# Kernel tuning notes

Hardware: AMD Instinct MI355X
Metric: run time of the kernel (lower is better)

The kernel has to match this reference:

```python
import jax, jax.numpy as jnp
import numpy as np

N, E, D = 50000, 600000, 128
NEG_SLOPE = 0.2

def setup_inputs() -> dict:
    key = jax.random.key(0)
    ks = jax.random.split(key, 12)
    s = 1.0 / np.sqrt(D)
    return {
        "x": jax.random.normal(ks[0], (N, D), jnp.float32),
        "edge_index": jax.random.randint(ks[1], (2, E), 0, N),
        "edge_attr": jax.random.normal(ks[2], (E, D), jnp.float32),
        "ln1_g": jnp.ones((D,), jnp.float32),
        "ln1_b": jnp.zeros((D,), jnp.float32),
        "W_lin": jax.random.normal(ks[3], (D, D), jnp.float32) * s,
        "att_src": jax.random.normal(ks[4], (D,), jnp.float32) * s,
        "att_dst": jax.random.normal(ks[5], (D,), jnp.float32) * s,
        "W_edge": jax.random.normal(ks[6], (D, D), jnp.float32) * s,
        "att_edge": jax.random.normal(ks[7], (D,), jnp.float32) * s,
        "gat_bias": jnp.zeros((D,), jnp.float32),
        "ln2_g": jnp.ones((D,), jnp.float32),
        "ln2_b": jnp.zeros((D,), jnp.float32),
        "W1": jax.random.normal(ks[8], (D, 4 * D), jnp.float32) * s,
        "b1": jnp.zeros((4 * D,), jnp.float32),
        "W2": jax.random.normal(ks[9], (4 * D, D), jnp.float32) * (1.0 / np.sqrt(4 * D)),
        "b2": jnp.zeros((D,), jnp.float32),
    }


def _layernorm(x, g, b, eps=1e-5):
    mu = jnp.mean(x, axis=-1, keepdims=True)
    var = jnp.mean(jnp.square(x - mu), axis=-1, keepdims=True)
    return (x - mu) * jax.lax.rsqrt(var + eps) * g + b


def _gat_conv(x, edge_index, edge_attr, W_lin, att_src, att_dst, W_edge, att_edge, gat_bias):
    # PyG GATConv, heads=1, concat=False, add_self_loops=False, edge_dim=D
    src, dst = edge_index[0], edge_index[1]
    h = x @ W_lin                      # [N, D] shared src/dst projection
    a_src = h @ att_src                # [N]
    a_dst = h @ att_dst                # [N]
    a_edge = (edge_attr @ W_edge) @ att_edge  # [E]
    alpha = a_src[src] + a_dst[dst] + a_edge  # [E]
    alpha = jnp.where(alpha > 0, alpha, NEG_SLOPE * alpha)  # leaky_relu(0.2)
    # segment softmax over destination nodes
    m = jax.ops.segment_max(alpha, dst, num_segments=N)
    m = jnp.where(jnp.isfinite(m), m, 0.0)
    ex = jnp.exp(alpha - m[dst])
    denom = jax.ops.segment_sum(ex, dst, num_segments=N)
    coef = ex / jnp.maximum(denom[dst], 1e-16)
    # weighted scatter-aggregation of source messages
    out = jax.ops.segment_sum(coef[:, None] * h[src], dst, num_segments=N)
    return out + gat_bias


def reference(x, edge_index, edge_attr, ln1_g, ln1_b, W_lin, att_src, att_dst,
              W_edge, att_edge, gat_bias, ln2_g, ln2_b, W1, b1, W2, b2):
    # pre-norm + GAT message passing + residual (dropout = eval identity)
    xn = _layernorm(x, ln1_g, ln1_b)
    x = x + _gat_conv(xn, edge_index, edge_attr, W_lin, att_src, att_dst,
                      W_edge, att_edge, gat_bias)
    # pre-norm + FFN + residual
    xn = _layernorm(x, ln2_g, ln2_b)
    ffn = jax.nn.relu(xn @ W1 + b1) @ W2 + b2
    return x + ffn
```

## Files before the change

### kernel.cpp

```cpp
#include <hip/hip_runtime.h>

#define D 128
#define NEG_SLOPE 0.2f

typedef __attribute__((ext_vector_type(8))) short short8;
typedef __attribute__((ext_vector_type(4))) float f32x4;

__device__ __forceinline__ float wred_sum(float v){
#pragma unroll
  for (int m = 32; m; m >>= 1) v += __shfl_xor(v, m);
  return v;
}
__device__ __forceinline__ int wred_sumi(int v){
#pragma unroll
  for (int m = 32; m; m >>= 1) v += __shfl_xor(v, m);
  return v;
}
__device__ __forceinline__ float wred_max(float v){
#pragma unroll
  for (int m = 32; m; m >>= 1) v = fmaxf(v, __shfl_xor(v, m));
  return v;
}
__device__ __forceinline__ unsigned short bf16r(float f){
  unsigned int u = __float_as_uint(f);
  u += 0x7fffu + ((u >> 16) & 1u);
  return (unsigned short)(u >> 16);
}
__device__ __forceinline__ float bf2f(unsigned int hi16){
  return __uint_as_float(hi16 << 16);
}

__global__ void k_prep0(const float* __restrict__ W_lin, const float* __restrict__ W1,
                        const float* __restrict__ W2, const float* __restrict__ W_edge,
                        const float* __restrict__ att_edge,
                        unsigned short* __restrict__ Wlt, unsigned short* __restrict__ W1t,
                        unsigned short* __restrict__ W2t, float* __restrict__ we,
                        int* __restrict__ cnt, int N){
  int t = blockIdx.x * blockDim.x + threadIdx.x;
  if (t < N) cnt[t] = 0;
  if (t < 128 * 128){
    int c = t >> 7, k = t & 127;
    Wlt[t] = bf16r(W_lin[k * 128 + c]);
  } else if (t < 128 * 128 + 512 * 128){
    int u = t - 128 * 128; int c = u >> 7, k = u & 127;
    W1t[u] = bf16r(W1[k * 512 + c]);
  } else if (t < 128 * 128 + 512 * 128 + 128 * 512){
    int u = t - (128 * 128 + 512 * 128); int c = u >> 9, k = u & 511;
    W2t[u] = bf16r(W2[k * 128 + c]);
  } else {
    int u = t - (128 * 128 + 512 * 128 + 128 * 512);
    if (u < 128){
      float s = 0.f;
      for (int j = 0; j < 128; ++j) s += W_edge[u * 128 + j] * att_edge[j];
      we[u] = s;
    }
  }
}

__global__ __launch_bounds__(256) void k_hgemm(const float* __restrict__ x,
                                               const unsigned short* __restrict__ Wlt,
                                               const float* __restrict__ ln1_g,
                                               const float* __restrict__ ln1_b,
                                               const float* __restrict__ att_src,
                                               const float* __restrict__ att_dst,
                                               const int* __restrict__ ei,
                                               unsigned short* __restrict__ hq,
                                               float* __restrict__ asrc,
                                               float* __restrict__ adst,
                                               int* __restrict__ cnt, int N, int E){
  int wid = threadIdx.x >> 6, lane = threadIdx.x & 63;
  int rb = blockIdx.x * 64 + wid * 16;
  int row = rb + (lane & 15);
  int rowc = row < N ? row : N - 1;
  int ksub = (lane >> 4) * 8;
  float v[4][8];
#pragma unroll
  for (int kb = 0; kb < 4; ++kb){
    float4 p0 = *(const float4*)(x + (size_t)rowc * 128 + kb * 32 + ksub);
    float4 p1 = *(const float4*)(x + (size_t)rowc * 128 + kb * 32 + ksub + 4);
    v[kb][0] = p0.x; v[kb][1] = p0.y; v[kb][2] = p0.z; v[kb][3] = p0.w;
    v[kb][4] = p1.x; v[kb][5] = p1.y; v[kb][6] = p1.z; v[kb][7] = p1.w;
  }
  float s = 0.f;
#pragma unroll
  for (int kb = 0; kb < 4; ++kb)
#pragma unroll
    for (int j = 0; j < 8; ++j) s += v[kb][j];
  s += __shfl_xor(s, 16); s += __shfl_xor(s, 32);
  float mu = s * (1.0f / 128.f);
  float q = 0.f;
#pragma unroll
  for (int kb = 0; kb < 4; ++kb)
#pragma unroll
    for (int j = 0; j < 8; ++j){ float d = v[kb][j] - mu; q += d * d; }
  q += __shfl_xor(q, 16); q += __shfl_xor(q, 32);
  float rstd = rsqrtf(q * (1.0f / 128.f) + 1e-5f);
  short8 a[4];
#pragma unroll
  for (int kb = 0; kb < 4; ++kb){
    float4 g0 = *(const float4*)(ln1_g + kb * 32 + ksub);
    float4 g1 = *(const float4*)(ln1_g + kb * 32 + ksub + 4);
    float4 b0 = *(const float4*)(ln1_b + kb * 32 + ksub);
    float4 b1 = *(const float4*)(ln1_b + kb * 32 + ksub + 4);
    float gg[8] = {g0.x,g0.y,g0.z,g0.w,g1.x,g1.y,g1.z,g1.w};
    float bb[8] = {b0.x,b0.y,b0.z,b0.w,b1.x,b1.y,b1.z,b1.w};
#pragma unroll
    for (int j = 0; j < 8; ++j)
      a[kb][j] = (short)bf16r((v[kb][j] - mu) * rstd * gg[j] + bb[j]);
  }
  f32x4 acc[8];
#pragma unroll
  for (int ct = 0; ct < 8; ++ct) acc[ct] = (f32x4){0.f, 0.f, 0.f, 0.f};
#pragma unroll
  for (int ct = 0; ct < 8; ++ct){
    int col = ct * 16 + (lane & 15);
#pragma unroll
    for (int kb = 0; kb < 4; ++kb){
      short8 bf = *(const short8*)(Wlt + (size_t)col * 128 + kb * 32 + ksub);
      acc[ct] = __builtin_amdgcn_mfma_f32_16x16x32_bf16(a[kb], bf, acc[ct], 0, 0, 0);
    }
  }
  int r0 = rb + (lane >> 4) * 4;
#pragma unroll
  for (int ct = 0; ct < 8; ++ct){
    int col = ct * 16 + (lane & 15);
#pragma unroll
    for (int j = 0; j < 4; ++j){
      int r = r0 + j;
      if (r < N) hq[(size_t)r * 128 + col] = bf16r(acc[ct][j]);
    }
  }
  float as_v[8], ad_v[8];
#pragma unroll
  for (int ct = 0; ct < 8; ++ct){
    int col = ct * 16 + (lane & 15);
    as_v[ct] = att_src[col];
    ad_v[ct] = att_dst[col];
  }
  float ps[4] = {0.f, 0.f, 0.f, 0.f}, pd[4] = {0.f, 0.f, 0.f, 0.f};
#pragma unroll
  for (int ct = 0; ct < 8; ++ct)
#pragma unroll
    for (int j = 0; j < 4; ++j){
      ps[j] += acc[ct][j] * as_v[ct];
      pd[j] += acc[ct][j] * ad_v[ct];
    }
#pragma unroll
  for (int m = 1; m < 16; m <<= 1)
#pragma unroll
    for (int j = 0; j < 4; ++j){
      ps[j] += __shfl_xor(ps[j], m);
      pd[j] += __shfl_xor(pd[j], m);
    }
  if ((lane & 15) == 0){
#pragma unroll
    for (int j = 0; j < 4; ++j){
      int r = r0 + j;
      if (r < N){ asrc[r] = ps[j]; adst[r] = pd[j]; }
    }
  }
  int t = blockIdx.x * blockDim.x + threadIdx.x;
  int stride = gridDim.x * blockDim.x;
  for (int e = t; e < E; e += stride) atomicAdd(&cnt[ei[E + e]], 1);
}

__global__ void k_escan(const int* __restrict__ cnt, int* __restrict__ start,
                        int* __restrict__ cursor, int N){
  int b = blockIdx.x, t = threadIdx.x;
  int base = b * 256;
  int acc = 0;
  for (int i = t; i < base; i += 256) acc += cnt[i];
  acc = wred_sumi(acc);
  __shared__ int wsum[4];
  if ((t & 63) == 0) wsum[t >> 6] = acc;
  __syncthreads();
  int s_off = wsum[0] + wsum[1] + wsum[2] + wsum[3];
  int i = base + t;
  int c = (i < N) ? cnt[i] : 0;
  __shared__ int sd[256];
  sd[t] = c;
  __syncthreads();
  for (int off = 1; off < 256; off <<= 1){
    int vv = (t >= off) ? sd[t - off] : 0;
    __syncthreads();
    sd[t] += vv;
    __syncthreads();
  }
  int st = s_off + sd[t] - c;
  if (i <= N) start[i] = st;
  if (i < N) cursor[i] = st;
}

__global__ void k_edge_scatter(const float* __restrict__ ea, const int* __restrict__ ei,
                               const float* __restrict__ we, const float* __restrict__ asrc,
                               const float* __restrict__ adst, int* __restrict__ cursor,
                               int2* __restrict__ esa, int E){
  int gw = (blockIdx.x * blockDim.x + threadIdx.x) >> 6;
  int lane = threadIdx.x & 63;
  int e = gw * 2 + (lane >> 5);
  int li = lane & 31;
  if (e >= E) return;
  float4 v = *(const float4*)(ea + (size_t)e * 128 + li * 4);
  float4 w = *(const float4*)(we + li * 4);
  float s = v.x * w.x + v.y * w.y + v.z * w.z + v.w * w.w;
#pragma unroll
  for (int m = 16; m; m >>= 1) s += __shfl_xor(s, m);
  if (li == 0){
    int sn = ei[e], dn = ei[E + e];
    float al = asrc[sn] + adst[dn] + s;
    al = al > 0.f ? al : NEG_SLOPE * al;
    int slot = atomicAdd(&cursor[dn], 1);
    esa[slot] = make_int2(sn, __float_as_int(al));
  }
}

__global__ void k_agg(const float* __restrict__ x, const unsigned short* __restrict__ hq,
                      const int* __restrict__ start, const int2* __restrict__ esa,
                      const float* __restrict__ gat_bias,
                      const float* __restrict__ g2, const float* __restrict__ b2,
                      float* __restrict__ out, unsigned short* __restrict__ xn2q, int N){
  int n = (blockIdx.x * blockDim.x + threadIdx.x) >> 6;
  int lane = threadIdx.x & 63;
  if (n >= N) return;
  int beg = start[n], end = start[n + 1];
  float m = -1e30f, ds = 0.f, a0 = 0.f, a1 = 0.f;
  for (int cb = beg; cb < end; cb += 64){
    int k = end - cb; if (k > 64) k = 64;
    int2 ev = (cb + lane < end) ? esa[cb + lane] : make_int2(0, (int)0xFF800000u);
    float al = __int_as_float(ev.y);
    float mn = fmaxf(m, wred_max(al));
    float sc = __expf(m - mn);
    ds *= sc; a0 *= sc; a1 *= sc;
    m = mn;
    float ex = __expf(al - m);
    int j = 0;
    for (; j + 4 <= k; j += 4){
      float e0 = __shfl(ex, j), e1 = __shfl(ex, j + 1);
      float e2 = __shfl(ex, j + 2), e3 = __shfl(ex, j + 3);
      int s0 = __shfl(ev.x, j), s1 = __shfl(ev.x, j + 1);
      int s2 = __shfl(ev.x, j + 2), s3 = __shfl(ev.x, j + 3);
      unsigned int h0 = *(const unsigned int*)(hq + (size_t)s0 * 128 + lane * 2);
      unsigned int h1 = *(const unsigned int*)(hq + (size_t)s1 * 128 + lane * 2);
      unsigned int h2 = *(const unsigned int*)(hq + (size_t)s2 * 128 + lane * 2);
      unsigned int h3 = *(const unsigned int*)(hq + (size_t)s3 * 128 + lane * 2);
      ds += e0 + e1 + e2 + e3;
      a0 += e0 * bf2f(h0 & 0xffffu) + e1 * bf2f(h1 & 0xffffu)
          + e2 * bf2f(h2 & 0xffffu) + e3 * bf2f(h3 & 0xffffu);
      a1 += e0 * bf2f(h0 >> 16) + e1 * bf2f(h1 >> 16)
          + e2 * bf2f(h2 >> 16) + e3 * bf2f(h3 >> 16);
    }
    for (; j < k; ++j){
      float ej = __shfl(ex, j);
      int sj = __shfl(ev.x, j);
      unsigned int hv = *(const unsigned int*)(hq + (size_t)sj * 128 + lane * 2);
      ds += ej;
      a0 += ej * bf2f(hv & 0xffffu);
      a1 += ej * bf2f(hv >> 16);
    }
  }
  float inv = (end > beg) ? 1.f / fmaxf(ds, 1e-16f) : 0.f;
  a0 *= inv; a1 *= inv;
  float2 xv  = *(const float2*)(x + (size_t)n * 128 + lane * 2);
  float2 gbv = *(const float2*)(gat_bias + lane * 2);
  float r0 = xv.x + a0 + gbv.x;
  float r1 = xv.y + a1 + gbv.y;
  float mu = wred_sum(r0 + r1) * (1.0f / 128.f);
  float d0 = r0 - mu, d1 = r1 - mu;
  float var = wred_sum(d0 * d0 + d1 * d1) * (1.0f / 128.f);
  float rstd = rsqrtf(var + 1e-5f);
  float2 gv = *(const float2*)(g2 + lane * 2);
  float2 bv = *(const float2*)(b2 + lane * 2);
  float o0 = d0 * rstd * gv.x + bv.x;
  float o1 = d1 * rstd * gv.y + bv.y;
  *(float2*)(out + (size_t)n * 128 + lane * 2) = make_float2(r0, r1);
  unsigned int p = (unsigned int)bf16r(o0) | ((unsigned int)bf16r(o1) << 16);
  *(unsigned int*)(xn2q + (size_t)n * 128 + lane * 2) = p;
}

__global__ __launch_bounds__(512) void k_ffn(const unsigned short* __restrict__ xn2q,
                                             const unsigned short* __restrict__ W1t,
                                             const unsigned short* __restrict__ W2t,
                                             const float* __restrict__ b1,
                                             const float* __restrict__ b2,
                                             float* __restrict__ out, int N){
  __shared__ unsigned short hid[64 * 512];
  int wid = threadIdx.x >> 6, lane = threadIdx.x & 63;
  int rg = wid >> 1;
  int ch = wid & 1;
  int rb = blockIdx.x * 64;
  int lr = rg * 16;
  int arow = rb + lr + (lane & 15);
  int arowc = arow < N ? arow : N - 1;
  int ksub = (lane >> 4) * 8;
  short8 a[4];
#pragma unroll
  for (int kb = 0; kb < 4; ++kb)
    a[kb] = *(const short8*)(xn2q + (size_t)arowc * 128 + kb * 32 + ksub);
  int lr0 = lr + (lane >> 4) * 4;
#pragma unroll 4
  for (int ct = 0; ct < 16; ++ct){
    int col = ch * 256 + ct * 16 + (lane & 15);
    f32x4 acc = {0.f, 0.f, 0.f, 0.f};
#pragma unroll
    for (int kb = 0; kb < 4; ++kb){
      short8 bf = *(const short8*)(W1t + (size_t)col * 128 + kb * 32 + ksub);
      acc = __builtin_amdgcn_mfma_f32_16x16x32_bf16(a[kb], bf, acc, 0, 0, 0);
    }
    float bias = b1[col];
#pragma unroll
    for (int j = 0; j < 4; ++j){
      float v = acc[j] + bias;
      v = v > 0.f ? v : 0.f;
      int row = lr0 + j;
      int byte = (col * 2) ^ ((row & 7) << 4);
      *(unsigned short*)((char*)hid + row * 1024 + byte) = bf16r(v);
    }
  }
  __syncthreads();
  f32x4 acc2[4];
#pragma unroll
  for (int ct = 0; ct < 4; ++ct) acc2[ct] = (f32x4){0.f, 0.f, 0.f, 0.f};
  int arow2 = lr + (lane & 15);
#pragma unroll 2
  for (int kb = 0; kb < 16; ++kb){
    int kbyte = (kb * 32 + ksub) * 2;
    int sb = kbyte ^ ((arow2 & 7) << 4);
    short8 af = *(const short8*)((const char*)hid + arow2 * 1024 + sb);
#pragma unroll
    for (int ct = 0; ct < 4; ++ct){
      int col = ch * 64 + ct * 16 + (lane & 15);
      short8 bf = *(const short8*)(W2t + (size_t)col * 512 + kb * 32 + ksub);
      acc2[ct] = __builtin_amdgcn_mfma_f32_16x16x32_bf16(af, bf, acc2[ct], 0, 0, 0);
    }
  }
  int r0 = rb + lr0;
#pragma unroll
  for (int ct = 0; ct < 4; ++ct){
    int col = ch * 64 + ct * 16 + (lane & 15);
    float bias = b2[col];
#pragma unroll
    for (int j = 0; j < 4; ++j){
      int row = r0 + j;
      if (row < N) out[(size_t)row * 128 + col] += acc2[ct][j] + bias;
    }
  }
}

extern "C" void kernel_launch(void* const* d_in, const int* in_sizes, int n_in,
                              void* d_out, int out_size, void* d_ws, size_t ws_size,
                              hipStream_t stream){
  const float* x        = (const float*)d_in[0];
  const int*   ei       = (const int*)  d_in[1];
  const float* ea       = (const float*)d_in[2];
  const float* ln1_g    = (const float*)d_in[3];
  const float* ln1_b    = (const float*)d_in[4];
  const float* W_lin    = (const float*)d_in[5];
  const float* att_src  = (const float*)d_in[6];
  const float* att_dst  = (const float*)d_in[7];
  const float* W_edge   = (const float*)d_in[8];
  const float* att_edge = (const float*)d_in[9];
  const float* gat_bias = (const float*)d_in[10];
  const float* ln2_g    = (const float*)d_in[11];
  const float* ln2_b    = (const float*)d_in[12];
  const float* W1       = (const float*)d_in[13];
  const float* b1       = (const float*)d_in[14];
  const float* W2       = (const float*)d_in[15];
  const float* b2       = (const float*)d_in[16];

  const int N = in_sizes[0] / 128;
  const int E = in_sizes[2] / 128;
  float* out = (float*)d_out;

  char* p = (char*)d_ws;
  auto carve = [&](size_t bytes) -> char* {
    char* r = p; p += (bytes + 255) & ~(size_t)255; return r;
  };
  unsigned short* hq       = (unsigned short*)carve((size_t)N * 128 * 2);
  unsigned short* xn2q     = (unsigned short*)carve((size_t)N * 128 * 2);
  float*          asrc     = (float*)carve((size_t)N * 4);
  float*          adst     = (float*)carve((size_t)N * 4);
  int2*           esa      = (int2*)carve((size_t)E * 8);
  int*            cnt      = (int*)carve((size_t)N * 4);
  int*            cursor   = (int*)carve((size_t)N * 4);
  int*            start    = (int*)carve((size_t)(N + 1) * 4);
  unsigned short* Wlt      = (unsigned short*)carve(128 * 128 * 2);
  unsigned short* W1t      = (unsigned short*)carve(512 * 128 * 2);
  unsigned short* W2t      = (unsigned short*)carve(128 * 512 * 2);
  float*          we       = (float*)carve(128 * 4);

  k_prep0<<<(128*128 + 512*128 + 128*512 + 128 + 255) / 256, 256, 0, stream>>>(
      W_lin, W1, W2, W_edge, att_edge, Wlt, W1t, W2t, we, cnt, N);
  k_hgemm<<<(N + 63) / 64, 256, 0, stream>>>(x, Wlt, ln1_g, ln1_b, att_src, att_dst, ei,
                                             hq, asrc, adst, cnt, N, E);
  k_escan<<<N / 256 + 1, 256, 0, stream>>>(cnt, start, cursor, N);
  k_edge_scatter<<<(E + 7) / 8, 256, 0, stream>>>(ea, ei, we, asrc, adst, cursor, esa, E);
  k_agg<<<(N + 3) / 4, 256, 0, stream>>>(x, hq, start, esa, gat_bias, ln2_g, ln2_b,
                                         out, xn2q, N);
  k_ffn<<<(N + 63) / 64, 512, 0, stream>>>(xn2q, W1t, W2t, b1, b2, out, N);
}
```

Measured before the change: 344.9 us.

## Fuse all GAT layer stages into one cooperative persistent kernel

Replaces the six-kernel pipeline with a single cooperative-launch persistent kernel that uses grid-wide syncs between phases: weight prep, edge-logit GEMV overlapped with the node GEMM on split block groups, a scan, the edge scatter, aggregation and the FFN. The goal is to remove launch gaps and tail idling between small kernels. The cost is a fixed grid of 256 blocks, a serial per-chunk scan prefix, and several grid barriers. Aggregation also switches to a two-pass max-then-sum softmax using half-warps per node, and the fallback k_agg gets the same two-pass loop.

After: 510.4 us. +48.0%, slower.

```diff
diff --git a/kernel.cpp b/kernel.cpp
--- a/kernel.cpp
+++ b/kernel.cpp
@@ -1,7 +1,13 @@
 #include <hip/hip_runtime.h>
+#include <hip/hip_cooperative_groups.h>
+
+namespace cg = cooperative_groups;
 
 #define D 128
 #define NEG_SLOPE 0.2f
+#define GRID 256
+#define BLK 512
+#define EB 160
 
 typedef __attribute__((ext_vector_type(8))) short short8;
 typedef __attribute__((ext_vector_type(4))) float f32x4;
@@ -29,6 +35,340 @@
 __device__ __forceinline__ float bf2f(unsigned int hi16){
   return __uint_as_float(hi16 << 16);
 }
+
+struct P {
+  const float *x; const int *ei; const float *ea;
+  const float *ln1_g, *ln1_b, *W_lin, *att_src, *att_dst, *W_edge, *att_edge;
+  const float *gat_bias, *ln2_g, *ln2_b, *W1, *b1, *W2, *b2;
+  float *out;
+  unsigned short *hq, *xn2q, *Wlt, *W1t, *W2t;
+  float *asrc, *adst, *we, *a_edge;
+  int2 *esa;
+  int *cnt, *cursor, *start;
+  int N, E;
+};
+
+__global__ __launch_bounds__(512) void k_mega(P p){
+  __shared__ unsigned short hid[64 * 512];
+  const int tid = threadIdx.x;
+  const int bid = blockIdx.x;
+  const int gtid = bid * BLK + tid;
+  const int GT = GRID * BLK;
+  cg::grid_group grd = cg::this_grid();
+
+  for (int i = gtid; i < p.N; i += GT) p.cnt[i] = 0;
+  for (int i = gtid; i < 128 * 128; i += GT){
+    int c = i >> 7, k = i & 127;
+    p.Wlt[i] = bf16r(p.W_lin[k * 128 + c]);
+  }
+  for (int i = gtid; i < 512 * 128; i += GT){
+    int c = i >> 7, k = i & 127;
+    p.W1t[i] = bf16r(p.W1[k * 512 + c]);
+  }
+  for (int i = gtid; i < 128 * 512; i += GT){
+    int c = i >> 9, k = i & 511;
+    p.W2t[i] = bf16r(p.W2[k * 128 + c]);
+  }
+  {
+    int hw = gtid >> 5, l32 = tid & 31;
+    if (hw < 128){
+      float4 wv = *(const float4*)(p.W_edge + hw * 128 + l32 * 4);
+      float4 av = *(const float4*)(p.att_edge + l32 * 4);
+      float s = wv.x * av.x + wv.y * av.y + wv.z * av.z + wv.w * av.w;
+#pragma unroll
+      for (int m = 16; m; m >>= 1) s += __shfl_xor(s, m);
+      if (l32 == 0) p.we[hw] = s;
+    }
+  }
+  grd.sync();
+
+  if (bid < EB){
+    int g = tid >> 3, l8 = tid & 7;
+    float4 w0 = *(const float4*)(p.we + l8 * 16);
+    float4 w1 = *(const float4*)(p.we + l8 * 16 + 4);
+    float4 w2 = *(const float4*)(p.we + l8 * 16 + 8);
+    float4 w3 = *(const float4*)(p.we + l8 * 16 + 12);
+    for (int e = bid * 64 + g; e < p.E; e += EB * 64){
+      const float4* row = (const float4*)(p.ea + (size_t)e * 128 + l8 * 16);
+      float4 v0 = row[0], v1 = row[1], v2 = row[2], v3 = row[3];
+      float s = v0.x*w0.x + v0.y*w0.y + v0.z*w0.z + v0.w*w0.w
+              + v1.x*w1.x + v1.y*w1.y + v1.z*w1.z + v1.w*w1.w
+              + v2.x*w2.x + v2.y*w2.y + v2.z*w2.z + v2.w*w2.w
+              + v3.x*w3.x + v3.y*w3.y + v3.z*w3.z + v3.w*w3.w;
+      s += __shfl_xor(s, 1); s += __shfl_xor(s, 2); s += __shfl_xor(s, 4);
+      if (l8 == 0) p.a_edge[e] = s;
+    }
+  } else {
+    int hb = bid - EB;
+    const int HB = GRID - EB;
+    int wid = tid >> 6, lane = tid & 63;
+    int T = (p.N + 127) >> 7;
+    int l15 = lane & 15, ksub = (lane >> 4) * 8;
+    for (int t = hb; t < T; t += HB){
+      int rb = t * 128 + wid * 16;
+      int row = rb + l15;
+      int rowc = row < p.N ? row : p.N - 1;
+      float v[4][8];
+#pragma unroll
+      for (int kb = 0; kb < 4; ++kb){
+        float4 p0 = *(const float4*)(p.x + (size_t)rowc * 128 + kb * 32 + ksub);
+        float4 p1 = *(const float4*)(p.x + (size_t)rowc * 128 + kb * 32 + ksub + 4);
+        v[kb][0]=p0.x; v[kb][1]=p0.y; v[kb][2]=p0.z; v[kb][3]=p0.w;
+        v[kb][4]=p1.x; v[kb][5]=p1.y; v[kb][6]=p1.z; v[kb][7]=p1.w;
+      }
+      float s = 0.f;
+#pragma unroll
+      for (int kb = 0; kb < 4; ++kb)
+#pragma unroll
+        for (int j = 0; j < 8; ++j) s += v[kb][j];
+      s += __shfl_xor(s, 16); s += __shfl_xor(s, 32);
+      float mu = s * (1.0f / 128.f);
+      float q = 0.f;
+#pragma unroll
+      for (int kb = 0; kb < 4; ++kb)
+#pragma unroll
+        for (int j = 0; j < 8; ++j){ float d = v[kb][j] - mu; q += d * d; }
+      q += __shfl_xor(q, 16); q += __shfl_xor(q, 32);
+      float rstd = rsqrtf(q * (1.0f / 128.f) + 1e-5f);
+      short8 a[4];
+#pragma unroll
+      for (int kb = 0; kb < 4; ++kb){
+        float4 g0 = *(const float4*)(p.ln1_g + kb * 32 + ksub);
+        float4 g1 = *(const float4*)(p.ln1_g + kb * 32 + ksub + 4);
+        float4 b0 = *(const float4*)(p.ln1_b + kb * 32 + ksub);
+        float4 b1 = *(const float4*)(p.ln1_b + kb * 32 + ksub + 4);
+        float gg[8] = {g0.x,g0.y,g0.z,g0.w,g1.x,g1.y,g1.z,g1.w};
+        float bb[8] = {b0.x,b0.y,b0.z,b0.w,b1.x,b1.y,b1.z,b1.w};
+#pragma unroll
+        for (int j = 0; j < 8; ++j)
+          a[kb][j] = (short)bf16r((v[kb][j] - mu) * rstd * gg[j] + bb[j]);
+      }
+      f32x4 acc[8];
+#pragma unroll
+      for (int ct = 0; ct < 8; ++ct) acc[ct] = (f32x4){0.f,0.f,0.f,0.f};
+#pragma unroll
+      for (int ct = 0; ct < 8; ++ct){
+        int col = ct * 16 + l15;
+#pragma unroll
+        for (int kb = 0; kb < 4; ++kb){
+          short8 bf = *(const short8*)(p.Wlt + (size_t)col * 128 + kb * 32 + ksub);
+          acc[ct] = __builtin_amdgcn_mfma_f32_16x16x32_bf16(a[kb], bf, acc[ct], 0, 0, 0);
+        }
+      }
+      int r0 = rb + (lane >> 4) * 4;
+#pragma unroll
+      for (int ct = 0; ct < 8; ++ct){
+        int col = ct * 16 + l15;
+#pragma unroll
+        for (int j = 0; j < 4; ++j){
+          int r = r0 + j;
+          if (r < p.N) p.hq[(size_t)r * 128 + col] = bf16r(acc[ct][j]);
+        }
+      }
+      float as_v[8], ad_v[8];
+#pragma unroll
+      for (int ct = 0; ct < 8; ++ct){
+        int col = ct * 16 + l15;
+        as_v[ct] = p.att_src[col];
+        ad_v[ct] = p.att_dst[col];
+      }
+      float ps[4] = {0,0,0,0}, pd[4] = {0,0,0,0};
+#pragma unroll
+      for (int ct = 0; ct < 8; ++ct)
+#pragma unroll
+        for (int j = 0; j < 4; ++j){
+          ps[j] += acc[ct][j] * as_v[ct];
+          pd[j] += acc[ct][j] * ad_v[ct];
+        }
+#pragma unroll
+      for (int m = 1; m < 16; m <<= 1)
+#pragma unroll
+        for (int j = 0; j < 4; ++j){
+          ps[j] += __shfl_xor(ps[j], m);
+          pd[j] += __shfl_xor(pd[j], m);
+        }
+      if (l15 == 0){
+#pragma unroll
+        for (int j = 0; j < 4; ++j){
+          int r = r0 + j;
+          if (r < p.N){ p.asrc[r] = ps[j]; p.adst[r] = pd[j]; }
+        }
+      }
+    }
+    for (int e = hb * BLK + tid; e < p.E; e += HB * BLK)
+      atomicAdd(&p.cnt[p.ei[p.E + e]], 1);
+  }
+  grd.sync();
+
+  {
+    int NC = (p.N + BLK) / BLK;
+    int* sd = (int*)hid;
+    int* wsum = sd + BLK;
+    for (int c = bid; c < NC; c += GRID){
+      int base = c * BLK;
+      int acc = 0;
+      for (int i = tid; i < base; i += BLK) acc += p.cnt[i];
+      acc = wred_sumi(acc);
+      if ((tid & 63) == 0) wsum[tid >> 6] = acc;
+      __syncthreads();
+      int s_off = 0;
+#pragma unroll
+      for (int w = 0; w < 8; ++w) s_off += wsum[w];
+      int i = base + tid;
+      int cv = (i < p.N) ? p.cnt[i] : 0;
+      sd[tid] = cv;
+      __syncthreads();
+      for (int off = 1; off < BLK; off <<= 1){
+        int vv = (tid >= off) ? sd[tid - off] : 0;
+        __syncthreads();
+        sd[tid] += vv;
+        __syncthreads();
+      }
+      int st = s_off + sd[tid] - cv;
+      if (i <= p.N) p.start[i] = st;
+      if (i < p.N)  p.cursor[i] = st;
+      __syncthreads();
+    }
+  }
+  grd.sync();
+
+  for (int e = gtid; e < p.E; e += GT){
+    int sn = p.ei[e], dn = p.ei[p.E + e];
+    float al = p.asrc[sn] + p.adst[dn] + p.a_edge[e];
+    al = al > 0.f ? al : NEG_SLOPE * al;
+    int slot = atomicAdd(&p.cursor[dn], 1);
+    p.esa[slot] = make_int2(sn, __float_as_int(al));
+  }
+  grd.sync();
+
+  {
+    int hw = tid >> 5, l32 = tid & 31;
+    for (int n = bid * 16 + hw; n < p.N; n += GRID * 16){
+      int beg = p.start[n], end = p.start[n + 1];
+      float m = -1e30f;
+      for (int i = beg + l32; i < end; i += 32)
+        m = fmaxf(m, __int_as_float(p.esa[i].y));
+#pragma unroll
+      for (int mm = 16; mm; mm >>= 1) m = fmaxf(m, __shfl_xor(m, mm));
+      float ds = 0.f, a0 = 0.f, a1 = 0.f, a2 = 0.f, a3 = 0.f;
+      int s = beg;
+      for (; s + 2 <= end; s += 2){
+        int2 e0 = p.esa[s], e1 = p.esa[s + 1];
+        float x0 = __expf(__int_as_float(e0.y) - m);
+        float x1 = __expf(__int_as_float(e1.y) - m);
+        uint2 h0 = *(const uint2*)(p.hq + (size_t)e0.x * 128 + l32 * 4);
+        uint2 h1 = *(const uint2*)(p.hq + (size_t)e1.x * 128 + l32 * 4);
+        ds += x0 + x1;
+        a0 += x0 * bf2f(h0.x & 0xffffu) + x1 * bf2f(h1.x & 0xffffu);
+        a1 += x0 * bf2f(h0.x >> 16)     + x1 * bf2f(h1.x >> 16);
+        a2 += x0 * bf2f(h0.y & 0xffffu) + x1 * bf2f(h1.y & 0xffffu);
+        a3 += x0 * bf2f(h0.y >> 16)     + x1 * bf2f(h1.y >> 16);
+      }
+      if (s < end){
+        int2 e0 = p.esa[s];
+        float x0 = __expf(__int_as_float(e0.y) - m);
+        uint2 h0 = *(const uint2*)(p.hq + (size_t)e0.x * 128 + l32 * 4);
+        ds += x0;
+        a0 += x0 * bf2f(h0.x & 0xffffu);
+        a1 += x0 * bf2f(h0.x >> 16);
+        a2 += x0 * bf2f(h0.y & 0xffffu);
+        a3 += x0 * bf2f(h0.y >> 16);
+      }
+      float inv = (end > beg) ? 1.f / fmaxf(ds, 1e-16f) : 0.f;
+      a0 *= inv; a1 *= inv; a2 *= inv; a3 *= inv;
+      float4 xv = *(const float4*)(p.x + (size_t)n * 128 + l32 * 4);
+      float4 gb = *(const float4*)(p.gat_bias + l32 * 4);
+      float r0 = xv.x + a0 + gb.x, r1 = xv.y + a1 + gb.y;
+      float r2 = xv.z + a2 + gb.z, r3 = xv.w + a3 + gb.w;
+      float sum = r0 + r1 + r2 + r3;
+#pragma unroll
+      for (int mm = 16; mm; mm >>= 1) sum += __shfl_xor(sum, mm);
+      float mu = sum * (1.0f / 128.f);
+      float d0 = r0 - mu, d1 = r1 - mu, d2 = r2 - mu, d3 = r3 - mu;
+      float q = d0*d0 + d1*d1 + d2*d2 + d3*d3;
+#pragma unroll
+      for (int mm = 16; mm; mm >>= 1) q += __shfl_xor(q, mm);
+      float rstd = rsqrtf(q * (1.0f / 128.f) + 1e-5f);
+      float4 gv = *(const float4*)(p.ln2_g + l32 * 4);
+      float4 bv = *(const float4*)(p.ln2_b + l32 * 4);
+      float o0 = d0*rstd*gv.x + bv.x, o1 = d1*rstd*gv.y + bv.y;
+      float o2 = d2*rstd*gv.z + bv.z, o3 = d3*rstd*gv.w + bv.w;
+      *(float4*)(p.out + (size_t)n * 128 + l32 * 4) = make_float4(r0, r1, r2, r3);
+      uint2 pk;
+      pk.x = (unsigned)bf16r(o0) | ((unsigned)bf16r(o1) << 16);
+      pk.y = (unsigned)bf16r(o2) | ((unsigned)bf16r(o3) << 16);
+      *(uint2*)(p.xn2q + (size_t)n * 128 + l32 * 4) = pk;
+    }
+  }
+  grd.sync();
+
+  {
+    int wid = tid >> 6, lane = tid & 63;
+    int rg = wid >> 1, ch = wid & 1;
+    int l15 = lane & 15, ksub = (lane >> 4) * 8;
+    int T = (p.N + 63) >> 6;
+    for (int t = bid; t < T; t += GRID){
+      int rb = t * 64;
+      int lr = rg * 16;
+      int arow = rb + lr + l15;
+      int arowc = arow < p.N ? arow : p.N - 1;
+      short8 a[4];
+#pragma unroll
+      for (int kb = 0; kb < 4; ++kb)
+        a[kb] = *(const short8*)(p.xn2q + (size_t)arowc * 128 + kb * 32 + ksub);
+      int lr0 = lr + (lane >> 4) * 4;
+#pragma unroll 4
+      for (int ct = 0; ct < 16; ++ct){
+        int col = ch * 256 + ct * 16 + l15;
+        f32x4 acc = {0.f, 0.f, 0.f, 0.f};
+#pragma unroll
+        for (int kb = 0; kb < 4; ++kb){
+          short8 bf = *(const short8*)(p.W1t + (size_t)col * 128 + kb * 32 + ksub);
+          acc = __builtin_amdgcn_mfma_f32_16x16x32_bf16(a[kb], bf, acc, 0, 0, 0);
+        }
+        float bias = p.b1[col];
+#pragma unroll
+        for (int j = 0; j < 4; ++j){
+          float v = acc[j] + bias;
+          v = v > 0.f ? v : 0.f;
+          int row = lr0 + j;
+          int byte = (col * 2) ^ ((row & 7) << 4);
+          *(unsigned short*)((char*)hid + row * 1024 + byte) = bf16r(v);
+        }
+      }
+      __syncthreads();
+      f32x4 acc2[4];
+#pragma unroll
+      for (int ct = 0; ct < 4; ++ct) acc2[ct] = (f32x4){0.f, 0.f, 0.f, 0.f};
+      int arow2 = lr + l15;
+#pragma unroll 2
+      for (int kb = 0; kb < 16; ++kb){
+        int kbyte = (kb * 32 + ksub) * 2;
+        int sb = kbyte ^ ((arow2 & 7) << 4);
+        short8 af = *(const short8*)((const char*)hid + arow2 * 1024 + sb);
+#pragma unroll
+        for (int ct = 0; ct < 4; ++ct){
+          int col = ch * 64 + ct * 16 + l15;
+          short8 bf = *(const short8*)(p.W2t + (size_t)col * 512 + kb * 32 + ksub);
+          acc2[ct] = __builtin_amdgcn_mfma_f32_16x16x32_bf16(af, bf, acc2[ct], 0, 0, 0);
+        }
+      }
+      int r0 = rb + lr0;
+#pragma unroll
+      for (int ct = 0; ct < 4; ++ct){
+        int col = ch * 64 + ct * 16 + l15;
+        float bias = p.b2[col];
+#pragma unroll
+        for (int j = 0; j < 4; ++j){
+          int row = r0 + j;
+          if (row < p.N) p.out[(size_t)row * 128 + col] += acc2[ct][j] + bias;
+        }
+      }
+      __syncthreads();
+    }
+  }
+}
+
 
 __global__ void k_prep0(const float* __restrict__ W_lin, const float* __restrict__ W1,
                         const float* __restrict__ W2, const float* __restrict__ W_edge,
@@ -78,8 +418,8 @@
   for (int kb = 0; kb < 4; ++kb){
     float4 p0 = *(const float4*)(x + (size_t)rowc * 128 + kb * 32 + ksub);
     float4 p1 = *(const float4*)(x + (size_t)rowc * 128 + kb * 32 + ksub + 4);
-    v[kb][0] = p0.x; v[kb][1] = p0.y; v[kb][2] = p0.z; v[kb][3] = p0.w;
-    v[kb][4] = p1.x; v[kb][5] = p1.y; v[kb][6] = p1.z; v[kb][7] = p1.w;
+    v[kb][0]=p0.x; v[kb][1]=p0.y; v[kb][2]=p0.z; v[kb][3]=p0.w;
+    v[kb][4]=p1.x; v[kb][5]=p1.y; v[kb][6]=p1.z; v[kb][7]=p1.w;
   }
   float s = 0.f;
 #pragma unroll
@@ -137,7 +477,7 @@
     as_v[ct] = att_src[col];
     ad_v[ct] = att_dst[col];
   }
-  float ps[4] = {0.f, 0.f, 0.f, 0.f}, pd[4] = {0.f, 0.f, 0.f, 0.f};
+  float ps[4] = {0.f,0.f,0.f,0.f}, pd[4] = {0.f,0.f,0.f,0.f};
 #pragma unroll
   for (int ct = 0; ct < 8; ++ct)
 #pragma unroll
@@ -223,40 +563,18 @@
   int lane = threadIdx.x & 63;
   if (n >= N) return;
   int beg = start[n], end = start[n + 1];
-  float m = -1e30f, ds = 0.f, a0 = 0.f, a1 = 0.f;
-  for (int cb = beg; cb < end; cb += 64){
-    int k = end - cb; if (k > 64) k = 64;
-    int2 ev = (cb + lane < end) ? esa[cb + lane] : make_int2(0, (int)0xFF800000u);
-    float al = __int_as_float(ev.y);
-    float mn = fmaxf(m, wred_max(al));
-    float sc = __expf(m - mn);
-    ds *= sc; a0 *= sc; a1 *= sc;
-    m = mn;
-    float ex = __expf(al - m);
-    int j = 0;
-    for (; j + 4 <= k; j += 4){
-      float e0 = __shfl(ex, j), e1 = __shfl(ex, j + 1);
-      float e2 = __shfl(ex, j + 2), e3 = __shfl(ex, j + 3);
-      int s0 = __shfl(ev.x, j), s1 = __shfl(ev.x, j + 1);
-      int s2 = __shfl(ev.x, j + 2), s3 = __shfl(ev.x, j + 3);
-      unsigned int h0 = *(const unsigned int*)(hq + (size_t)s0 * 128 + lane * 2);
-      unsigned int h1 = *(const unsigned int*)(hq + (size_t)s1 * 128 + lane * 2);
-      unsigned int h2 = *(const unsigned int*)(hq + (size_t)s2 * 128 + lane * 2);
-      unsigned int h3 = *(const unsigned int*)(hq + (size_t)s3 * 128 + lane * 2);
-      ds += e0 + e1 + e2 + e3;
-      a0 += e0 * bf2f(h0 & 0xffffu) + e1 * bf2f(h1 & 0xffffu)
-          + e2 * bf2f(h2 & 0xffffu) + e3 * bf2f(h3 & 0xffffu);
-      a1 += e0 * bf2f(h0 >> 16) + e1 * bf2f(h1 >> 16)
-          + e2 * bf2f(h2 >> 16) + e3 * bf2f(h3 >> 16);
-    }
-    for (; j < k; ++j){
-      float ej = __shfl(ex, j);
-      int sj = __shfl(ev.x, j);
-      unsigned int hv = *(const unsigned int*)(hq + (size_t)sj * 128 + lane * 2);
-      ds += ej;
-      a0 += ej * bf2f(hv & 0xffffu);
-      a1 += ej * bf2f(hv >> 16);
-    }
+  float m = -1e30f;
+  for (int i = beg + lane; i < end; i += 64) m = fmaxf(m, __int_as_float(esa[i].y));
+  m = wred_max(m);
+  float ds = 0.f, a0 = 0.f, a1 = 0.f;
+#pragma unroll 2
+  for (int s = beg; s < end; ++s){
+    int2 ev = esa[s];
+    float ex = __expf(__int_as_float(ev.y) - m);
+    ds += ex;
+    unsigned int hv = *(const unsigned int*)(hq + (size_t)ev.x * 128 + lane * 2);
+    a0 += ex * bf2f(hv & 0xffffu);
+    a1 += ex * bf2f(hv >> 16);
   }
   float inv = (end > beg) ? 1.f / fmaxf(ds, 1e-16f) : 0.f;
   a0 *= inv; a1 *= inv;
@@ -273,8 +591,8 @@
   float o0 = d0 * rstd * gv.x + bv.x;
   float o1 = d1 * rstd * gv.y + bv.y;
   *(float2*)(out + (size_t)n * 128 + lane * 2) = make_float2(r0, r1);
-  unsigned int p = (unsigned int)bf16r(o0) | ((unsigned int)bf16r(o1) << 16);
-  *(unsigned int*)(xn2q + (size_t)n * 128 + lane * 2) = p;
+  unsigned int pk = (unsigned int)bf16r(o0) | ((unsigned int)bf16r(o1) << 16);
+  *(unsigned int*)(xn2q + (size_t)n * 128 + lane * 2) = pk;
 }
 
 __global__ __launch_bounds__(512) void k_ffn(const unsigned short* __restrict__ xn2q,
@@ -371,30 +689,50 @@
   const int E = in_sizes[2] / 128;
   float* out = (float*)d_out;
 
-  char* p = (char*)d_ws;
+  char* pp = (char*)d_ws;
   auto carve = [&](size_t bytes) -> char* {
-    char* r = p; p += (bytes + 255) & ~(size_t)255; return r;
+    char* r = pp; pp += (bytes + 255) & ~(size_t)255; return r;
   };
-  unsigned short* hq       = (unsigned short*)carve((size_t)N * 128 * 2);
-  unsigned short* xn2q     = (unsigned short*)carve((size_t)N * 128 * 2);
-  float*          asrc     = (float*)carve((size_t)N * 4);
-  float*          adst     = (float*)carve((size_t)N * 4);
-  int2*           esa      = (int2*)carve((size_t)E * 8);
-  int*            cnt      = (int*)carve((size_t)N * 4);
-  int*            cursor   = (int*)carve((size_t)N * 4);
-  int*            start    = (int*)carve((size_t)(N + 1) * 4);
-  unsigned short* Wlt      = (unsigned short*)carve(128 * 128 * 2);
-  unsigned short* W1t      = (unsigned short*)carve(512 * 128 * 2);
-  unsigned short* W2t      = (unsigned short*)carve(128 * 512 * 2);
-  float*          we       = (float*)carve(128 * 4);
-
-  k_prep0<<<(128*128 + 512*128 + 128*512 + 128 + 255) / 256, 256, 0, stream>>>(
-      W_lin, W1, W2, W_edge, att_edge, Wlt, W1t, W2t, we, cnt, N);
-  k_hgemm<<<(N + 63) / 64, 256, 0, stream>>>(x, Wlt, ln1_g, ln1_b, att_src, att_dst, ei,
-                                             hq, asrc, adst, cnt, N, E);
-  k_escan<<<N / 256 + 1, 256, 0, stream>>>(cnt, start, cursor, N);
-  k_edge_scatter<<<(E + 7) / 8, 256, 0, stream>>>(ea, ei, we, asrc, adst, cursor, esa, E);
-  k_agg<<<(N + 3) / 4, 256, 0, stream>>>(x, hq, start, esa, gat_bias, ln2_g, ln2_b,
-                                         out, xn2q, N);
-  k_ffn<<<(N + 63) / 64, 512, 0, stream>>>(xn2q, W1t, W2t, b1, b2, out, N);
-}
+  unsigned short* hq     = (unsigned short*)carve((size_t)N * 128 * 2);
+  unsigned short* xn2q   = (unsigned short*)carve((size_t)N * 128 * 2);
+  float*          asrc   = (float*)carve((size_t)N * 4);
+  float*          adst   = (float*)carve((size_t)N * 4);
+  int2*           esa    = (int2*)carve((size_t)E * 8);
+  float*          a_edge = (float*)carve((size_t)E * 4);
+  int*            cnt    = (int*)carve((size_t)N * 4);
+  int*            cursor = (int*)carve((size_t)N * 4);
+  int*            start  = (int*)carve((size_t)(N + 1) * 4);
+  unsigned short* Wlt    = (unsigned short*)carve(128 * 128 * 2);
+  unsigned short* W1t    = (unsigned short*)carve(512 * 128 * 2);
+  unsigned short* W2t    = (unsigned short*)carve(128 * 512 * 2);
+  float*          we     = (float*)carve(128 * 4);
+
+  P prm;
+  prm.x = x; prm.ei = ei; prm.ea = ea;
+  prm.ln1_g = ln1_g; prm.ln1_b = ln1_b; prm.W_lin = W_lin;
+  prm.att_src = att_src; prm.att_dst = att_dst;
+  prm.W_edge = W_edge; prm.att_edge = att_edge;
+  prm.gat_bias = gat_bias; prm.ln2_g = ln2_g; prm.ln2_b = ln2_b;
+  prm.W1 = W1; prm.b1 = b1; prm.W2 = W2; prm.b2 = b2;
+  prm.out = out;
+  prm.hq = hq; prm.xn2q = xn2q; prm.Wlt = Wlt; prm.W1t = W1t; prm.W2t = W2t;
+  prm.asrc = asrc; prm.adst = adst; prm.we = we; prm.a_edge = a_edge;
+  prm.esa = esa; prm.cnt = cnt; prm.cursor = cursor; prm.start = start;
+  prm.N = N; prm.E = E;
+
+  void* args[] = { (void*)&prm };
+  hipError_t err = hipLaunchCooperativeKernel((const void*)k_mega, dim3(GRID), dim3(BLK),
+                                              args, 0, stream);
+  if (err != hipSuccess){
+    (void)hipGetLastError();
+    k_prep0<<<(128*128 + 512*128 + 128*512 + 128 + 255) / 256, 256, 0, stream>>>(
+        W_lin, W1, W2, W_edge, att_edge, Wlt, W1t, W2t, we, cnt, N);
+    k_hgemm<<<(N + 63) / 64, 256, 0, stream>>>(x, Wlt, ln1_g, ln1_b, att_src, att_dst, ei,
+                                               hq, asrc, adst, cnt, N, E);
+    k_escan<<<N / 256 + 1, 256, 0, stream>>>(cnt, start, cursor, N);
+    k_edge_scatter<<<(E + 7) / 8, 256, 0, stream>>>(ea, ei, we, asrc, adst, cursor, esa, E);
+    k_agg<<<(N + 3) / 4, 256, 0, stream>>>(x, hq, start, esa, gat_bias, ln2_g, ln2_b,
+                                           out, xn2q, N);
+    k_ffn<<<(N + 63) / 64, 512, 0, stream>>>(xn2q, W1t, W2t, b1, b2, out, N);
+  }
+}
```
